# Optimization experiments

Hardware: AMD Instinct MI355X
Metric: run time of the kernel (lower is better)

Reference implementation:

```python
import jax, jax.numpy as jnp
import numpy as np

N_NODES = 50000
N_EDGES = 800000
D = 128
BN_EPS = 1e-5

def setup_inputs() -> dict:
    key = jax.random.key(0)
    k1, k2, k3, k4, k5 = jax.random.split(key, 5)
    features = jax.random.normal(k1, (N_NODES, D), dtype=jnp.float32)
    W = jax.random.normal(k2, (D, D), dtype=jnp.float32) * (1.0 / np.sqrt(D))
    b = jax.random.normal(k3, (D,), dtype=jnp.float32) * 0.01
    gamma = jnp.ones((D,), dtype=jnp.float32)
    beta = jnp.zeros((D,), dtype=jnp.float32)
    edge_src = jax.random.randint(k4, (N_EDGES,), 0, N_NODES, dtype=jnp.int32)
    edge_dst = jax.random.randint(k5, (N_EDGES,), 0, N_NODES, dtype=jnp.int32)
    return {"features": features, "W": W, "b": b, "gamma": gamma,
            "beta": beta, "edge_src": edge_src, "edge_dst": edge_dst}

def reference(features, W, b, gamma, beta, edge_src, edge_dst):
    h_in = features
    # in-degrees per node, clamped to >= 1
    degs = jax.ops.segment_sum(jnp.ones_like(edge_dst, dtype=jnp.float32),
                               edge_dst, num_segments=N_NODES)
    norm = jnp.clip(degs, 1.0, None) ** -0.5  # [N]
    norm = norm[:, None]                       # [N, 1]
    # symmetric-norm GCN: scale, copy_src + sum reduce, linear apply, scale
    x = features * norm
    agg = jax.ops.segment_sum(x[edge_src], edge_dst, num_segments=N_NODES)  # [N, D]
    h = agg @ W.T + b
    h = h * norm
    # BatchNorm1d (training-mode math: batch stats over nodes, biased var)
    mean = jnp.mean(h, axis=0)
    var = jnp.mean((h - mean) ** 2, axis=0)
    h = (h - mean) * jax.lax.rsqrt(var + BN_EPS) * gamma + beta
    # ReLU activation, residual; dropout is identity in eval
    h = jax.nn.relu(h)
    h = h_in + h
    return h
```

## Files before the change

### kernel.cpp

```cpp
#include <hip/hip_runtime.h>

#define D 128
#define BN_EPS 1e-5f
#define NPART 8
#define NCHUNK 256
#define CAP 64
#define NBKT 16

typedef __attribute__((ext_vector_type(8))) short short8;
typedef __attribute__((ext_vector_type(4))) float f32x4;

__device__ __forceinline__ unsigned short f2bf(float f) {
    unsigned int x = __float_as_uint(f);
    return (unsigned short)((x + 0x7fffu + ((x >> 16) & 1u)) >> 16);
}

__device__ __forceinline__ void atomAddF(float* p, float v) {
    unsafeAtomicAdd(p, v);
}

__global__ __launch_bounds__(256) void k_prep(
        const int* __restrict__ src, const int* __restrict__ dst,
        int* __restrict__ cnt, unsigned short* __restrict__ srcs,
        int nE, int PS, int CH,
        const float4* __restrict__ inA, ushort4* __restrict__ outA, int n4a,
        const float4* __restrict__ inB, ushort4* __restrict__ outB, int n4b) {
    int bid = blockIdx.x;
    if (bid < NPART * NCHUNK) {
        int p = bid & (NPART - 1);
        int c = bid >> 3;
        unsigned lo = (unsigned)(p * PS);
        int e0 = c * CH;
        int e1 = min(e0 + CH, nE);
        for (int e = e0 + (int)threadIdx.x; e < e1; e += 1024) {
            int ea = e, eb = e + 256, ec = e + 512, ed = e + 768;
            int d0 = dst[ea];
            int d1 = (eb < e1) ? dst[eb] : 0;
            int d2 = (ec < e1) ? dst[ec] : 0;
            int d3 = (ed < e1) ? dst[ed] : 0;
            bool a0 = (unsigned)d0 - lo < (unsigned)PS;
            bool a1 = (eb < e1) && ((unsigned)d1 - lo < (unsigned)PS);
            bool a2 = (ec < e1) && ((unsigned)d2 - lo < (unsigned)PS);
            bool a3 = (ed < e1) && ((unsigned)d3 - lo < (unsigned)PS);
            int s0 = a0 ? atomicAdd(&cnt[d0], 1) : CAP;
            int s1 = a1 ? atomicAdd(&cnt[d1], 1) : CAP;
            int s2 = a2 ? atomicAdd(&cnt[d2], 1) : CAP;
            int s3 = a3 ? atomicAdd(&cnt[d3], 1) : CAP;
            if (s0 < CAP) srcs[(size_t)d0 * CAP + s0] = (unsigned short)src[ea];
            if (s1 < CAP) srcs[(size_t)d1 * CAP + s1] = (unsigned short)src[eb];
            if (s2 < CAP) srcs[(size_t)d2 * CAP + s2] = (unsigned short)src[ec];
            if (s3 < CAP) srcs[(size_t)d3 * CAP + s3] = (unsigned short)src[ed];
        }
    } else {
        int i = (bid - NPART * NCHUNK) * 256 + threadIdx.x;
        const float4* in; ushort4* out; int k;
        if (i < n4a) { in = inA; out = outA; k = i; }
        else { k = i - n4a; if (k >= n4b) return; in = inB; out = outB; }
        float4 v = in[k];
        ushort4 o;
        o.x = f2bf(v.x); o.y = f2bf(v.y); o.z = f2bf(v.z); o.w = f2bf(v.w);
        out[k] = o;
    }
}

template <bool FB>
__global__ __launch_bounds__(256) void k_gather(const int* __restrict__ cnt,
                                                const unsigned short* __restrict__ srcs,
                                                const void* __restrict__ featp,
                                                unsigned int* __restrict__ aggout,
                                                int nN) {
    int node = (blockIdx.x * 256 + threadIdx.x) >> 5;
    if (node >= nN) return;
    int l = threadIdx.x & 31;

    int end = cnt[node];
    if (end > CAP) end = CAP;
    const unsigned short* sl = srcs + (size_t)node * CAP;

    float a0 = 0.0f, a1 = 0.0f, a2 = 0.0f, a3 = 0.0f;
    int i = 0;

    if (FB) {
        const uint2* fb = (const uint2*)featp + l;
        for (; i + 3 < end; i += 4) {
            int s0 = sl[i], s1 = sl[i + 1], s2 = sl[i + 2], s3 = sl[i + 3];
            float n0 = rsqrtf(fmaxf((float)cnt[s0], 1.0f));
            float n1 = rsqrtf(fmaxf((float)cnt[s1], 1.0f));
            float n2 = rsqrtf(fmaxf((float)cnt[s2], 1.0f));
            float n3 = rsqrtf(fmaxf((float)cnt[s3], 1.0f));
            uint2 u0 = fb[(size_t)s0 * 32], u1 = fb[(size_t)s1 * 32];
            uint2 u2 = fb[(size_t)s2 * 32], u3 = fb[(size_t)s3 * 32];
            a0 += __uint_as_float(u0.x << 16) * n0 + __uint_as_float(u1.x << 16) * n1
                + __uint_as_float(u2.x << 16) * n2 + __uint_as_float(u3.x << 16) * n3;
            a1 += __uint_as_float(u0.x & 0xffff0000u) * n0 + __uint_as_float(u1.x & 0xffff0000u) * n1
                + __uint_as_float(u2.x & 0xffff0000u) * n2 + __uint_as_float(u3.x & 0xffff0000u) * n3;
            a2 += __uint_as_float(u0.y << 16) * n0 + __uint_as_float(u1.y << 16) * n1
                + __uint_as_float(u2.y << 16) * n2 + __uint_as_float(u3.y << 16) * n3;
            a3 += __uint_as_float(u0.y & 0xffff0000u) * n0 + __uint_as_float(u1.y & 0xffff0000u) * n1
                + __uint_as_float(u2.y & 0xffff0000u) * n2 + __uint_as_float(u3.y & 0xffff0000u) * n3;
        }
        for (; i < end; ++i) {
            int s = sl[i];
            float n = rsqrtf(fmaxf((float)cnt[s], 1.0f));
            uint2 u = fb[(size_t)s * 32];
            a0 += __uint_as_float(u.x << 16) * n;
            a1 += __uint_as_float(u.x & 0xffff0000u) * n;
            a2 += __uint_as_float(u.y << 16) * n;
            a3 += __uint_as_float(u.y & 0xffff0000u) * n;
        }
    } else {
        const float4* fb = (const float4*)featp + l;
        for (; i + 3 < end; i += 4) {
            int s0 = sl[i], s1 = sl[i + 1], s2 = sl[i + 2], s3 = sl[i + 3];
            float n0 = rsqrtf(fmaxf((float)cnt[s0], 1.0f));
            float n1 = rsqrtf(fmaxf((float)cnt[s1], 1.0f));
            float n2 = rsqrtf(fmaxf((float)cnt[s2], 1.0f));
            float n3 = rsqrtf(fmaxf((float)cnt[s3], 1.0f));
            float4 f0 = fb[(size_t)s0 * 32], f1 = fb[(size_t)s1 * 32];
            float4 f2 = fb[(size_t)s2 * 32], f3 = fb[(size_t)s3 * 32];
            a0 += f0.x * n0 + f1.x * n1 + f2.x * n2 + f3.x * n3;
            a1 += f0.y * n0 + f1.y * n1 + f2.y * n2 + f3.y * n3;
            a2 += f0.z * n0 + f1.z * n1 + f2.z * n2 + f3.z * n3;
            a3 += f0.w * n0 + f1.w * n1 + f2.w * n2 + f3.w * n3;
        }
        for (; i < end; ++i) {
            int s = sl[i];
            float n = rsqrtf(fmaxf((float)cnt[s], 1.0f));
            float4 f = fb[(size_t)s * 32];
            a0 += f.x * n; a1 += f.y * n; a2 += f.z * n; a3 += f.w * n;
        }
    }
    uint2 packed;
    packed.x = (unsigned int)f2bf(a0) | ((unsigned int)f2bf(a1) << 16);
    packed.y = (unsigned int)f2bf(a2) | ((unsigned int)f2bf(a3) << 16);
    ((uint2*)aggout)[(size_t)node * 64 + 32 + l] = packed;
}

__global__ __launch_bounds__(256) void k_gemm(
        const unsigned short* __restrict__ Adata,
        const unsigned short* __restrict__ Wbf,
        const float* __restrict__ b,
        const int* __restrict__ cnt,
        float* __restrict__ h,
        float* __restrict__ colpart,
        int nN) {
    const int tid = threadIdx.x;
    const int lane = tid & 63;
    const int wv = tid >> 6;
    const int wcol0 = wv * 32;
    const int l15 = lane & 15;
    const int lq = lane >> 4;
    const int row0 = blockIdx.x * 64;

    __shared__ float tp[4][16 * 36];

    short8 bfrag[2][4];
    #pragma unroll
    for (int ct = 0; ct < 2; ++ct) {
        int n = wcol0 + ct * 16 + l15;
        #pragma unroll
        for (int kc = 0; kc < 4; ++kc)
            bfrag[ct][kc] = *(const short8*)(Wbf + n * 128 + kc * 32 + lq * 8);
    }
    const float bc0 = b[wcol0 + l15], bc1 = b[wcol0 + 16 + l15];

    short8 afrag[4][4];
    #pragma unroll
    for (int rt = 0; rt < 4; ++rt) {
        int arow = row0 + rt * 16 + l15;
        int arc = arow < nN ? arow : (nN - 1);
        #pragma unroll
        for (int kc = 0; kc < 4; ++kc)
            afrag[rt][kc] = *(const short8*)(Adata + (size_t)arc * 256 + 128 + kc * 32 + lq * 8);
    }
    __syncthreads();

    float s1[2] = {0.0f, 0.0f}, s2[2] = {0.0f, 0.0f};
    const int sub = lane & 3;
    const int r16 = lane >> 2;

    #pragma unroll
    for (int rt = 0; rt < 4; ++rt) {
        int r0 = row0 + rt * 16;
        f32x4 acc0 = {0.0f, 0.0f, 0.0f, 0.0f};
        f32x4 acc1 = {0.0f, 0.0f, 0.0f, 0.0f};
        #pragma unroll
        for (int kc = 0; kc < 4; ++kc) {
            acc0 = __builtin_amdgcn_mfma_f32_16x16x32_bf16(afrag[rt][kc], bfrag[0][kc], acc0, 0, 0, 0);
            acc1 = __builtin_amdgcn_mfma_f32_16x16x32_bf16(afrag[rt][kc], bfrag[1][kc], acc1, 0, 0, 0);
        }

        #pragma unroll
        for (int reg = 0; reg < 4; ++reg) {
            int row = r0 + lq * 4 + reg;
            float nm = 0.0f;
            if (row < nN) nm = rsqrtf(fmaxf((float)cnt[row], 1.0f));
            float v0 = (acc0[reg] + bc0) * nm;
            float v1 = (acc1[reg] + bc1) * nm;
            int lrow = lq * 4 + reg;
            tp[wv][lrow * 36 + l15]      = v0;
            tp[wv][lrow * 36 + 16 + l15] = v1;
            if (row < nN) {
                s1[0] += v0; s2[0] += v0 * v0;
                s1[1] += v1; s2[1] += v1 * v1;
            }
        }
        int row = r0 + r16;
        if (row < nN) {
            float4 t0 = *(const float4*)&tp[wv][r16 * 36 + sub * 4];
            float4 t1 = *(const float4*)&tp[wv][r16 * 36 + 16 + sub * 4];
            size_t base = (size_t)row * 128 + wcol0 + sub * 4;
            *(float4*)(h + base) = t0;
            *(float4*)(h + base + 16) = t1;
        }
    }

    #pragma unroll
    for (int ct = 0; ct < 2; ++ct) {
        s1[ct] += __shfl_xor(s1[ct], 16, 64);
        s1[ct] += __shfl_xor(s1[ct], 32, 64);
        s2[ct] += __shfl_xor(s2[ct], 16, 64);
        s2[ct] += __shfl_xor(s2[ct], 32, 64);
    }
    const int bkt = blockIdx.x & (NBKT - 1);
    if (lane < 16) {
        atomAddF(&colpart[(wcol0 + lane) * NBKT + bkt], s1[0]);
        atomAddF(&colpart[(128 + wcol0 + lane) * NBKT + bkt], s2[0]);
        atomAddF(&colpart[(wcol0 + 16 + lane) * NBKT + bkt], s1[1]);
        atomAddF(&colpart[(128 + wcol0 + 16 + lane) * NBKT + bkt], s2[1]);
    }
}

__global__ __launch_bounds__(256) void k_bn_out(const float* __restrict__ colpart,
                                                const float* __restrict__ gamma,
                                                const float* __restrict__ beta,
                                                float* __restrict__ h,
                                                const float* __restrict__ feat,
                                                float inv_n, int total4) {
    __shared__ float sc[128], sh[128];
    int tid = threadIdx.x;
    if (tid < 128) {
        float s = 0.0f, q = 0.0f;
        #pragma unroll
        for (int j = 0; j < NBKT; ++j) {
            s += colpart[tid * NBKT + j];
            q += colpart[(128 + tid) * NBKT + j];
        }
        float mean = s * inv_n;
        float var = q * inv_n - mean * mean;
        float scv = gamma[tid] * rsqrtf(var + BN_EPS);
        sc[tid] = scv;
        sh[tid] = beta[tid] - mean * scv;
    }
    __syncthreads();
    int t = blockIdx.x * 256 + tid;
    if (t >= total4) return;
    int base = t * 4;
    int j = base & 127;
    float4 hv = *(const float4*)(h + base);
    float4 fv = *(const float4*)(feat + base);
    float4 o;
    o.x = fv.x + fmaxf(hv.x * sc[j + 0] + sh[j + 0], 0.0f);
    o.y = fv.y + fmaxf(hv.y * sc[j + 1] + sh[j + 1], 0.0f);
    o.z = fv.z + fmaxf(hv.z * sc[j + 2] + sh[j + 2], 0.0f);
    o.w = fv.w + fmaxf(hv.w * sc[j + 3] + sh[j + 3], 0.0f);
    *(float4*)(h + base) = o;
}

extern "C" void kernel_launch(void* const* d_in, const int* in_sizes, int n_in,
                              void* d_out, int out_size, void* d_ws, size_t ws_size,
                              hipStream_t stream) {
    const float* feat  = (const float*)d_in[0];
    const float* W     = (const float*)d_in[1];
    const float* b     = (const float*)d_in[2];
    const float* gamma = (const float*)d_in[3];
    const float* beta  = (const float*)d_in[4];
    const int* esrc = (const int*)d_in[5];
    const int* edst = (const int*)d_in[6];

    const int nN = in_sizes[0] / D;
    const int nE = in_sizes[5];
    const int PS = (nN + NPART - 1) / NPART;
    const int CH = (nE + NCHUNK - 1) / NCHUNK;

    float* h = (float*)d_out;

    unsigned short* Wbf    = (unsigned short*)d_ws;
    unsigned short* srcs   = Wbf + 128 * 128;
    int*            cnt    = (int*)(srcs + (size_t)nN * CAP);
    float*          colpart= (float*)(cnt + nN);
    unsigned short* featbf = (unsigned short*)(colpart + 256 * NBKT);

    size_t need_full = (size_t)((char*)(featbf + (size_t)nN * D) - (char*)d_ws);
    bool useFB = ws_size >= need_full;

    hipMemsetAsync(cnt, 0, ((size_t)nN + 256 * NBKT + 64) * sizeof(int), stream);

    int n4a = 128 * 128 / 4;
    int n4b = useFB ? nN * D / 4 : 0;
    int castBlocks = (n4a + n4b + 255) / 256;
    k_prep<<<NPART * NCHUNK + castBlocks, 256, 0, stream>>>(
        esrc, edst, cnt, srcs, nE, PS, CH,
        (const float4*)W, (ushort4*)Wbf, n4a,
        (const float4*)feat, (ushort4*)featbf, n4b);

    int gblocks = (nN * 32 + 255) / 256;
    if (useFB)
        k_gather<true><<<gblocks, 256, 0, stream>>>(cnt, srcs, featbf, (unsigned int*)d_out, nN);
    else
        k_gather<false><<<gblocks, 256, 0, stream>>>(cnt, srcs, feat, (unsigned int*)d_out, nN);

    int gb = (nN + 63) / 64;
    float inv_n = 1.0f / (float)nN;

    k_gemm<<<gb, 256, 0, stream>>>((const unsigned short*)d_out, Wbf, b, cnt,
                                   h, colpart, nN);

    int total4 = nN * D / 4;
    k_bn_out<<<(total4 + 255) / 256, 256, 0, stream>>>(colpart, gamma, beta,
                                                       h, feat, inv_n, total4);
}
```

Before: 210.5 us.

## Fuse neighbor gather into GEMM kernel via LDS-staged bf16 tile

Merges the gather and GEMM kernels: each block of 64 nodes aggregates its neighbor features into a bf16 tile in LDS, then runs the MFMA GEMM directly from shared memory. This removes the global write and re-read of the aggregated matrix and one kernel launch. The gather loop now issues 8 independent feature loads per iteration instead of 4, and the edge-bucketing prep loop unrolls to 8 edges per thread. The trade-off is that each wave handles 8 nodes serially, so there is less parallelism in the gather phase and more LDS use per block.

```diff
diff --git a/kernel.cpp b/kernel.cpp
--- a/kernel.cpp
+++ b/kernel.cpp
@@ -32,24 +32,23 @@
         unsigned lo = (unsigned)(p * PS);
         int e0 = c * CH;
         int e1 = min(e0 + CH, nE);
-        for (int e = e0 + (int)threadIdx.x; e < e1; e += 1024) {
-            int ea = e, eb = e + 256, ec = e + 512, ed = e + 768;
-            int d0 = dst[ea];
-            int d1 = (eb < e1) ? dst[eb] : 0;
-            int d2 = (ec < e1) ? dst[ec] : 0;
-            int d3 = (ed < e1) ? dst[ed] : 0;
-            bool a0 = (unsigned)d0 - lo < (unsigned)PS;
-            bool a1 = (eb < e1) && ((unsigned)d1 - lo < (unsigned)PS);
-            bool a2 = (ec < e1) && ((unsigned)d2 - lo < (unsigned)PS);
-            bool a3 = (ed < e1) && ((unsigned)d3 - lo < (unsigned)PS);
-            int s0 = a0 ? atomicAdd(&cnt[d0], 1) : CAP;
-            int s1 = a1 ? atomicAdd(&cnt[d1], 1) : CAP;
-            int s2 = a2 ? atomicAdd(&cnt[d2], 1) : CAP;
-            int s3 = a3 ? atomicAdd(&cnt[d3], 1) : CAP;
-            if (s0 < CAP) srcs[(size_t)d0 * CAP + s0] = (unsigned short)src[ea];
-            if (s1 < CAP) srcs[(size_t)d1 * CAP + s1] = (unsigned short)src[eb];
-            if (s2 < CAP) srcs[(size_t)d2 * CAP + s2] = (unsigned short)src[ec];
-            if (s3 < CAP) srcs[(size_t)d3 * CAP + s3] = (unsigned short)src[ed];
+        for (int e = e0 + (int)threadIdx.x; e < e1; e += 2048) {
+            int dd[8]; bool aa[8]; int ss[8];
+            #pragma unroll
+            for (int t = 0; t < 8; ++t) {
+                int idx = e + t * 256;
+                bool in = idx < e1;
+                int d = in ? dst[idx] : 0;
+                dd[t] = d;
+                aa[t] = in && ((unsigned)d - lo < (unsigned)PS);
+            }
+            #pragma unroll
+            for (int t = 0; t < 8; ++t)
+                ss[t] = aa[t] ? atomicAdd(&cnt[dd[t]], 1) : CAP;
+            #pragma unroll
+            for (int t = 0; t < 8; ++t)
+                if (ss[t] < CAP)
+                    srcs[(size_t)dd[t] * CAP + ss[t]] = (unsigned short)src[e + t * 256];
         }
     } else {
         int i = (bid - NPART * NCHUNK) * 256 + threadIdx.x;
@@ -64,95 +63,99 @@
 }
 
 template <bool FB>
-__global__ __launch_bounds__(256) void k_gather(const int* __restrict__ cnt,
-                                                const unsigned short* __restrict__ srcs,
-                                                const void* __restrict__ featp,
-                                                unsigned int* __restrict__ aggout,
-                                                int nN) {
-    int node = (blockIdx.x * 256 + threadIdx.x) >> 5;
-    if (node >= nN) return;
-    int l = threadIdx.x & 31;
-
-    int end = cnt[node];
-    if (end > CAP) end = CAP;
-    const unsigned short* sl = srcs + (size_t)node * CAP;
-
-    float a0 = 0.0f, a1 = 0.0f, a2 = 0.0f, a3 = 0.0f;
-    int i = 0;
-
-    if (FB) {
-        const uint2* fb = (const uint2*)featp + l;
-        for (; i + 3 < end; i += 4) {
-            int s0 = sl[i], s1 = sl[i + 1], s2 = sl[i + 2], s3 = sl[i + 3];
-            float n0 = rsqrtf(fmaxf((float)cnt[s0], 1.0f));
-            float n1 = rsqrtf(fmaxf((float)cnt[s1], 1.0f));
-            float n2 = rsqrtf(fmaxf((float)cnt[s2], 1.0f));
-            float n3 = rsqrtf(fmaxf((float)cnt[s3], 1.0f));
-            uint2 u0 = fb[(size_t)s0 * 32], u1 = fb[(size_t)s1 * 32];
-            uint2 u2 = fb[(size_t)s2 * 32], u3 = fb[(size_t)s3 * 32];
-            a0 += __uint_as_float(u0.x << 16) * n0 + __uint_as_float(u1.x << 16) * n1
-                + __uint_as_float(u2.x << 16) * n2 + __uint_as_float(u3.x << 16) * n3;
-            a1 += __uint_as_float(u0.x & 0xffff0000u) * n0 + __uint_as_float(u1.x & 0xffff0000u) * n1
-                + __uint_as_float(u2.x & 0xffff0000u) * n2 + __uint_as_float(u3.x & 0xffff0000u) * n3;
-            a2 += __uint_as_float(u0.y << 16) * n0 + __uint_as_float(u1.y << 16) * n1
-                + __uint_as_float(u2.y << 16) * n2 + __uint_as_float(u3.y << 16) * n3;
-            a3 += __uint_as_float(u0.y & 0xffff0000u) * n0 + __uint_as_float(u1.y & 0xffff0000u) * n1
-                + __uint_as_float(u2.y & 0xffff0000u) * n2 + __uint_as_float(u3.y & 0xffff0000u) * n3;
-        }
-        for (; i < end; ++i) {
-            int s = sl[i];
-            float n = rsqrtf(fmaxf((float)cnt[s], 1.0f));
-            uint2 u = fb[(size_t)s * 32];
-            a0 += __uint_as_float(u.x << 16) * n;
-            a1 += __uint_as_float(u.x & 0xffff0000u) * n;
-            a2 += __uint_as_float(u.y << 16) * n;
-            a3 += __uint_as_float(u.y & 0xffff0000u) * n;
-        }
-    } else {
-        const float4* fb = (const float4*)featp + l;
-        for (; i + 3 < end; i += 4) {
-            int s0 = sl[i], s1 = sl[i + 1], s2 = sl[i + 2], s3 = sl[i + 3];
-            float n0 = rsqrtf(fmaxf((float)cnt[s0], 1.0f));
-            float n1 = rsqrtf(fmaxf((float)cnt[s1], 1.0f));
-            float n2 = rsqrtf(fmaxf((float)cnt[s2], 1.0f));
-            float n3 = rsqrtf(fmaxf((float)cnt[s3], 1.0f));
-            float4 f0 = fb[(size_t)s0 * 32], f1 = fb[(size_t)s1 * 32];
-            float4 f2 = fb[(size_t)s2 * 32], f3 = fb[(size_t)s3 * 32];
-            a0 += f0.x * n0 + f1.x * n1 + f2.x * n2 + f3.x * n3;
-            a1 += f0.y * n0 + f1.y * n1 + f2.y * n2 + f3.y * n3;
-            a2 += f0.z * n0 + f1.z * n1 + f2.z * n2 + f3.z * n3;
-            a3 += f0.w * n0 + f1.w * n1 + f2.w * n2 + f3.w * n3;
-        }
-        for (; i < end; ++i) {
-            int s = sl[i];
-            float n = rsqrtf(fmaxf((float)cnt[s], 1.0f));
-            float4 f = fb[(size_t)s * 32];
-            a0 += f.x * n; a1 += f.y * n; a2 += f.z * n; a3 += f.w * n;
-        }
-    }
-    uint2 packed;
-    packed.x = (unsigned int)f2bf(a0) | ((unsigned int)f2bf(a1) << 16);
-    packed.y = (unsigned int)f2bf(a2) | ((unsigned int)f2bf(a3) << 16);
-    ((uint2*)aggout)[(size_t)node * 64 + 32 + l] = packed;
-}
-
-__global__ __launch_bounds__(256) void k_gemm(
-        const unsigned short* __restrict__ Adata,
+__global__ __launch_bounds__(256, 2) void k_gg(
+        const int* __restrict__ cnt,
+        const unsigned short* __restrict__ srcs,
+        const void* __restrict__ featp,
         const unsigned short* __restrict__ Wbf,
         const float* __restrict__ b,
-        const int* __restrict__ cnt,
         float* __restrict__ h,
         float* __restrict__ colpart,
         int nN) {
+    __shared__ unsigned short Ald[64 * 136];
+    __shared__ float tp[4][16 * 36];
+
     const int tid = threadIdx.x;
+    const int row0 = blockIdx.x * 64;
+
+    {
+        const int hw = tid >> 5;
+        const int l = tid & 31;
+        for (int j = 0; j < 8; ++j) {
+            int local = hw * 8 + j;
+            int node = row0 + local;
+            float a0 = 0.0f, a1 = 0.0f, a2 = 0.0f, a3 = 0.0f;
+            if (node < nN) {
+                int end = cnt[node];
+                if (end > CAP) end = CAP;
+                const unsigned short* sl = srcs + (size_t)node * CAP;
+                int i = 0;
+                if (FB) {
+                    const uint2* fb = (const uint2*)featp + l;
+                    for (; i + 7 < end; i += 8) {
+                        int s[8];
+                        #pragma unroll
+                        for (int t = 0; t < 8; ++t) s[t] = sl[i + t];
+                        uint2 u[8];
+                        #pragma unroll
+                        for (int t = 0; t < 8; ++t) u[t] = fb[(size_t)s[t] * 32];
+                        float nm[8];
+                        #pragma unroll
+                        for (int t = 0; t < 8; ++t)
+                            nm[t] = rsqrtf(fmaxf((float)cnt[s[t]], 1.0f));
+                        #pragma unroll
+                        for (int t = 0; t < 8; ++t) {
+                            a0 += __uint_as_float(u[t].x << 16) * nm[t];
+                            a1 += __uint_as_float(u[t].x & 0xffff0000u) * nm[t];
+                            a2 += __uint_as_float(u[t].y << 16) * nm[t];
+                            a3 += __uint_as_float(u[t].y & 0xffff0000u) * nm[t];
+                        }
+                    }
+                    for (; i < end; ++i) {
+                        int s = sl[i];
+                        float nm = rsqrtf(fmaxf((float)cnt[s], 1.0f));
+                        uint2 u = fb[(size_t)s * 32];
+                        a0 += __uint_as_float(u.x << 16) * nm;
+                        a1 += __uint_as_float(u.x & 0xffff0000u) * nm;
+                        a2 += __uint_as_float(u.y << 16) * nm;
+                        a3 += __uint_as_float(u.y & 0xffff0000u) * nm;
+                    }
+                } else {
+                    const float4* fb = (const float4*)featp + l;
+                    for (; i + 3 < end; i += 4) {
+                        int s0 = sl[i], s1 = sl[i + 1], s2 = sl[i + 2], s3 = sl[i + 3];
+                        float n0 = rsqrtf(fmaxf((float)cnt[s0], 1.0f));
+                        float n1 = rsqrtf(fmaxf((float)cnt[s1], 1.0f));
+                        float n2 = rsqrtf(fmaxf((float)cnt[s2], 1.0f));
+                        float n3 = rsqrtf(fmaxf((float)cnt[s3], 1.0f));
+                        float4 f0 = fb[(size_t)s0 * 32], f1 = fb[(size_t)s1 * 32];
+                        float4 f2 = fb[(size_t)s2 * 32], f3 = fb[(size_t)s3 * 32];
+                        a0 += f0.x * n0 + f1.x * n1 + f2.x * n2 + f3.x * n3;
+                        a1 += f0.y * n0 + f1.y * n1 + f2.y * n2 + f3.y * n3;
+                        a2 += f0.z * n0 + f1.z * n1 + f2.z * n2 + f3.z * n3;
+                        a3 += f0.w * n0 + f1.w * n1 + f2.w * n2 + f3.w * n3;
+                    }
+                    for (; i < end; ++i) {
+                        int s = sl[i];
+                        float nm = rsqrtf(fmaxf((float)cnt[s], 1.0f));
+                        float4 f = fb[(size_t)s * 32];
+                        a0 += f.x * nm; a1 += f.y * nm; a2 += f.z * nm; a3 += f.w * nm;
+                    }
+                }
+            }
+            uint2 packed;
+            packed.x = (unsigned int)f2bf(a0) | ((unsigned int)f2bf(a1) << 16);
+            packed.y = (unsigned int)f2bf(a2) | ((unsigned int)f2bf(a3) << 16);
+            *(uint2*)&Ald[local * 136 + l * 4] = packed;
+        }
+    }
+    __syncthreads();
+
     const int lane = tid & 63;
     const int wv = tid >> 6;
     const int wcol0 = wv * 32;
     const int l15 = lane & 15;
     const int lq = lane >> 4;
-    const int row0 = blockIdx.x * 64;
-
-    __shared__ float tp[4][16 * 36];
 
     short8 bfrag[2][4];
     #pragma unroll
@@ -164,17 +167,6 @@
     }
     const float bc0 = b[wcol0 + l15], bc1 = b[wcol0 + 16 + l15];
 
-    short8 afrag[4][4];
-    #pragma unroll
-    for (int rt = 0; rt < 4; ++rt) {
-        int arow = row0 + rt * 16 + l15;
-        int arc = arow < nN ? arow : (nN - 1);
-        #pragma unroll
-        for (int kc = 0; kc < 4; ++kc)
-            afrag[rt][kc] = *(const short8*)(Adata + (size_t)arc * 256 + 128 + kc * 32 + lq * 8);
-    }
-    __syncthreads();
-
     float s1[2] = {0.0f, 0.0f}, s2[2] = {0.0f, 0.0f};
     const int sub = lane & 3;
     const int r16 = lane >> 2;
@@ -182,12 +174,17 @@
     #pragma unroll
     for (int rt = 0; rt < 4; ++rt) {
         int r0 = row0 + rt * 16;
+        short8 af[4];
+        #pragma unroll
+        for (int kc = 0; kc < 4; ++kc)
+            af[kc] = *(const short8*)(Ald + (rt * 16 + l15) * 136 + kc * 32 + lq * 8);
+
         f32x4 acc0 = {0.0f, 0.0f, 0.0f, 0.0f};
         f32x4 acc1 = {0.0f, 0.0f, 0.0f, 0.0f};
         #pragma unroll
         for (int kc = 0; kc < 4; ++kc) {
-            acc0 = __builtin_amdgcn_mfma_f32_16x16x32_bf16(afrag[rt][kc], bfrag[0][kc], acc0, 0, 0, 0);
-            acc1 = __builtin_amdgcn_mfma_f32_16x16x32_bf16(afrag[rt][kc], bfrag[1][kc], acc1, 0, 0, 0);
+            acc0 = __builtin_amdgcn_mfma_f32_16x16x32_bf16(af[kc], bfrag[0][kc], acc0, 0, 0, 0);
+            acc1 = __builtin_amdgcn_mfma_f32_16x16x32_bf16(af[kc], bfrag[1][kc], acc1, 0, 0, 0);
         }
 
         #pragma unroll
@@ -304,19 +301,14 @@
         (const float4*)W, (ushort4*)Wbf, n4a,
         (const float4*)feat, (ushort4*)featbf, n4b);
 
-    int gblocks = (nN * 32 + 255) / 256;
+    int gb = (nN + 63) / 64;
     if (useFB)
-        k_gather<true><<<gblocks, 256, 0, stream>>>(cnt, srcs, featbf, (unsigned int*)d_out, nN);
+        k_gg<true><<<gb, 256, 0, stream>>>(cnt, srcs, featbf, Wbf, b, h, colpart, nN);
     else
-        k_gather<false><<<gblocks, 256, 0, stream>>>(cnt, srcs, feat, (unsigned int*)d_out, nN);
-
-    int gb = (nN + 63) / 64;
+        k_gg<false><<<gb, 256, 0, stream>>>(cnt, srcs, feat, Wbf, b, h, colpart, nN);
+
+    int total4 = nN * D / 4;
     float inv_n = 1.0f / (float)nN;
-
-    k_gemm<<<gb, 256, 0, stream>>>((const unsigned short*)d_out, Wbf, b, cnt,
-                                   h, colpart, nN);
-
-    int total4 = nN * D / 4;
     k_bn_out<<<(total4 + 255) / 256, 256, 0, stream>>>(colpart, gamma, beta,
                                                        h, feat, inv_n, total4);
 }
```

Measured after the change: 214.0 us. No clear change (+1.7%).
